# Kernel optimization log

Measured on AMD Instinct MI355X. Metric: run time of the kernel, lower is better.

The kernel has to match this reference:

```python
import jax, jax.numpy as jnp
import numpy as np

EMBED_DIM = 1024
NUM_HEADS = 16
HEAD_DIM = EMBED_DIM // NUM_HEADS
B, S = 4, 2048


def setup_inputs() -> dict:
    key = jax.random.key(0)
    k1, k2, k3, k4, k5 = jax.random.split(key, 5)
    x = jax.random.normal(k1, (B, S, EMBED_DIM), dtype=jnp.float32)
    # torch nn.Linear params: W [out, in], b [out]; init scale ~ 1/sqrt(in)
    s = 1.0 / np.sqrt(EMBED_DIM)
    qkv_w = jax.random.uniform(k2, (3 * EMBED_DIM, EMBED_DIM), jnp.float32, -s, s)
    qkv_b = jax.random.uniform(k3, (3 * EMBED_DIM,), jnp.float32, -s, s)
    out_w = jax.random.uniform(k4, (EMBED_DIM, EMBED_DIM), jnp.float32, -s, s)
    out_b = jax.random.uniform(k5, (EMBED_DIM,), jnp.float32, -s, s)
    return {"x": x, "qkv_w": qkv_w, "qkv_b": qkv_b, "out_w": out_w, "out_b": out_b}


def reference(x, qkv_w, qkv_b, out_w, out_b):
    b, s, e = x.shape
    # qkv: [B,S,3E]
    qkv = x @ qkv_w.T + qkv_b
    # Faithful to source: reshape to [B,S,H,3*hd] then transpose -> [B,H,S,3*hd]
    qkv = qkv.reshape(b, s, NUM_HEADS, 3 * HEAD_DIM).transpose(0, 2, 1, 3)
    q, k, v = jnp.split(qkv, 3, axis=-1)  # each [B,H,S,hd]
    q = q / np.sqrt(HEAD_DIM).astype(np.float32)
    scores = jnp.einsum('bhqd,bhkd->bhqk', q, k)  # [B,H,S,S]
    attn = jax.nn.softmax(scores, axis=-1)
    out = jnp.einsum('bhqk,bhkd->bhqd', attn, v)  # [B,H,S,hd]
    out = out.transpose(0, 2, 1, 3).reshape(b, s, e)
    return out @ out_w.T + out_b
```

## Files before the change

### kernel.cpp

```cpp
#include <hip/hip_runtime.h>

#define EMBED   1024
#define THREE_E 3072
#define NHEAD   16
#define HDIM    64
#define BATCH   4
#define SEQ     2048
#define MTOK    (BATCH * SEQ)
#define QKW     2048

typedef __attribute__((ext_vector_type(8))) _Float16 half8;
typedef __attribute__((ext_vector_type(4))) _Float16 half4;
typedef __attribute__((ext_vector_type(4))) float    f32x4;

#define QSCALE 0.18033688011112042f

__device__ inline f32x4 mfma16(half8 a, half8 b, f32x4 c) {
    return __builtin_amdgcn_mfma_f32_16x16x32_f16(a, b, c, 0, 0, 0);
}
__device__ inline f32x4 mfma16k16(half4 a, half4 b, f32x4 c) {
    return __builtin_amdgcn_mfma_f32_16x16x16f16(a, b, c, 0, 0, 0);
}

__device__ inline float exp2x(float x) {
    float r;
    asm("v_exp_f32 %0, %1" : "=v"(r) : "v"(x));
    return r;
}

__device__ inline void gld16(const void* g, void* l) {
    __builtin_amdgcn_global_load_lds(
        (const __attribute__((address_space(1))) unsigned*)g,
        (__attribute__((address_space(3))) unsigned*)l, 16, 0, 0);
}

__global__ __launch_bounds__(256) void tohi_kernel(const float* __restrict__ in,
                                                   _Float16* __restrict__ hi, int n)
{
    int i = (blockIdx.x * 256 + threadIdx.x) << 2;
    if (i < n) {
        const float4 v = *(const float4*)(in + i);
        half4 h;
        h[0] = (_Float16)v.x; h[1] = (_Float16)v.y;
        h[2] = (_Float16)v.z; h[3] = (_Float16)v.w;
        *(half4*)(hi + i) = h;
    }
}

template<int OMODE>
__global__ __launch_bounds__(256) void gemm_mfma_nt(
    const _Float16* __restrict__ Ahi,
    const _Float16* __restrict__ Bhi,
    const float*  __restrict__ bias,
    float* __restrict__ Cf,
    _Float16* __restrict__ QKhi,
    _Float16* __restrict__ Vthi,
    int N, int K)
{
    __shared__ __align__(16) _Float16 sA[2][8][64][8];
    __shared__ __align__(16) _Float16 sB[2][8][64][8];

    const int tid  = threadIdx.x;
    const int w    = tid >> 6;
    const int lane = tid & 63;
    const int quad = lane >> 4;
    const int c    = lane & 15;
    const int wm   = w >> 1, wn = w & 1;

    const int gx   = gridDim.x;
    const int nwg  = gx * gridDim.y;
    const int lin0 = blockIdx.y * gx + blockIdx.x;
    const int wg   = (lin0 & 7) * (nwg >> 3) + (lin0 >> 3);
    const int m0   = (wg / gx) << 7;
    const int n0   = (wg % gx) << 7;

    f32x4 acc[4][4];
#pragma unroll
    for (int i = 0; i < 4; ++i)
#pragma unroll
        for (int j = 0; j < 4; ++j) acc[i][j] = (f32x4){0.f, 0.f, 0.f, 0.f};

    const _Float16* ap0 = Ahi + (size_t)(m0 + (w << 4)       + c) * K + (quad << 3);
    const _Float16* ap1 = Ahi + (size_t)(m0 + ((4 + w) << 4) + c) * K + (quad << 3);
    const _Float16* bp0 = Bhi + (size_t)(n0 + (w << 4)       + c) * K + (quad << 3);
    const _Float16* bp1 = Bhi + (size_t)(n0 + ((4 + w) << 4) + c) * K + (quad << 3);

    auto stage = [&](int bfs) {
        gld16(ap0, &sA[bfs][w][0][0]);
        gld16(ap1, &sA[bfs][4 + w][0][0]);
        gld16(bp0, &sB[bfs][w][0][0]);
        gld16(bp1, &sB[bfs][4 + w][0][0]);
        ap0 += 32; ap1 += 32; bp0 += 32; bp1 += 32;
    };

    stage(0);
    int bf = 0;
    for (int k0 = 0; k0 < K; k0 += 32) {
        __syncthreads();
        if (k0 + 32 < K) stage(bf ^ 1);

        half8 aH[4], bH[4];
#pragma unroll
        for (int i = 0; i < 4; ++i) {
            aH[i] = *(const half8*)&sA[bf][(wm << 2) + i][lane][0];
            bH[i] = *(const half8*)&sB[bf][(wn << 2) + i][lane][0];
        }
#pragma unroll
        for (int i = 0; i < 4; ++i)
#pragma unroll
            for (int j = 0; j < 4; ++j)
                acc[i][j] = mfma16(aH[i], bH[j], acc[i][j]);
        bf ^= 1;
    }

#pragma unroll
    for (int j = 0; j < 4; ++j) {
        const int n  = n0 + (wn << 6) + (j << 4) + c;
        const float bb = bias[n];
        const int h  = n / 192;
        const int rem = n - h * 192;
#pragma unroll
        for (int i = 0; i < 4; ++i) {
            const int mb = m0 + (wm << 6) + (i << 4) + (quad << 2);
            if constexpr (OMODE == 0) {
#pragma unroll
                for (int r = 0; r < 4; ++r)
                    Cf[(size_t)(mb + r) * N + n] = acc[i][j][r] + bb;
            } else {
                if (rem < 128) {
                    const size_t col = h * 128 + rem;
                    const float scale = (rem < 64) ? QSCALE : 1.0f;
#pragma unroll
                    for (int r = 0; r < 4; ++r)
                        QKhi[(size_t)(mb + r) * QKW + col] =
                            (_Float16)((acc[i][j][r] + bb) * scale);
                } else {
                    const int d = rem - 128;
                    const int b = mb >> 11;
                    const int s = mb & 2047;
                    half4 h4;
#pragma unroll
                    for (int r = 0; r < 4; ++r)
                        h4[r] = (_Float16)(acc[i][j][r] + bb);
                    const size_t off = ((size_t)(h * 64 + d) * BATCH + b) * SEQ + s;
                    *(half4*)(Vthi + off) = h4;
                }
            }
        }
    }
}

__global__ __launch_bounds__(256, 4) void attn_mfma(
    const _Float16* __restrict__ qkhi,
    const _Float16* __restrict__ vthi,
    _Float16* __restrict__ attnf)
{
    __shared__ __align__(16) _Float16 Kf[2][8][512];
    __shared__ __align__(16) _Float16 Vf[2][8][512];

    const int tid  = threadIdx.x;
    const int w    = tid >> 6;
    const int lane = tid & 63;
    const int quad = lane >> 4;
    const int c    = lane & 15;

    const int lin = blockIdx.x;
    const int g   = lin & 7;
    const int s   = lin >> 3;
    const int bh  = g * 8 + (s >> 4);
    const int qt  = s & 15;
    const int b   = bh >> 4, h = bh & 15;
    const int q0  = qt * 128;

    const size_t bSEQ  = (size_t)b * SEQ;
    const int    qcol  = h * 128;
    const int    kcol  = h * 128 + 64;
    const size_t vbase = ((size_t)(h * 64) * BATCH + b) * SEQ;

    half8 qh[2][2];
#pragma unroll
    for (int t = 0; t < 2; ++t) {
        const size_t row = (bSEQ + q0 + w * 32 + t * 16 + c) * QKW;
#pragma unroll
        for (int ks = 0; ks < 2; ++ks)
            qh[t][ks] = *(const half8*)(qkhi + row + qcol + ks * 32 + quad * 8);
    }

    f32x4 lacc[2];
    f32x4 oacc[4][2];
#pragma unroll
    for (int t = 0; t < 2; ++t) {
        lacc[t] = (f32x4){0.f, 0.f, 0.f, 0.f};
#pragma unroll
        for (int v = 0; v < 4; ++v) oacc[v][t] = (f32x4){0.f, 0.f, 0.f, 0.f};
    }

    const half4 one4 = {(_Float16)1.f, (_Float16)1.f, (_Float16)1.f, (_Float16)1.f};

    const int ku0 = w >> 1,       kks0 = w & 1;
    const int ku1 = (4 + w) >> 1, kks1 = (4 + w) & 1;
    const _Float16* kp0 = qkhi + (bSEQ + ku0 * 16 + c) * QKW + kcol + kks0 * 32 + quad * 8;
    const _Float16* kp1 = qkhi + (bSEQ + ku1 * 16 + c) * QKW + kcol + kks1 * 32 + quad * 8;
    const int lswz = lane ^ ((((lane >> 3) & 1) << 1) | (((lane >> 4) & 1) << 2));
    const int qs   = lswz >> 4, cs = lswz & 15;
    const _Float16* vp0 = vthi + vbase + (size_t)(ku0 * 16 + cs) * (BATCH * SEQ) + kks0 * 32 + qs * 8;
    const _Float16* vp1 = vthi + vbase + (size_t)(ku1 * 16 + cs) * (BATCH * SEQ) + kks1 * 32 + qs * 8;

    auto stageKV = [&](int bfs) {
        gld16(kp0, &Kf[bfs][w][0]);
        gld16(kp1, &Kf[bfs][4 + w][0]);
        gld16(vp0, &Vf[bfs][w][0]);
        gld16(vp1, &Vf[bfs][4 + w][0]);
        kp0 += 64 * QKW; kp1 += 64 * QKW; vp0 += 64; vp1 += 64;
    };

    stageKV(0);
    int bf = 0;

    for (int kt = 0; kt < SEQ / 64; ++kt) {
        __syncthreads();
        if (kt + 1 < SEQ / 64) stageKV(bf ^ 1);

        f32x4 sacc[2][4];
        __builtin_amdgcn_s_setprio(1);
#pragma unroll
        for (int u = 0; u < 4; ++u) {
            const half8 kh0 = *(const half8*)&Kf[bf][(u << 1) + 0][lane << 3];
            const half8 kh1 = *(const half8*)&Kf[bf][(u << 1) + 1][lane << 3];
#pragma unroll
            for (int t = 0; t < 2; ++t) {
                f32x4 a = (f32x4){0.f, 0.f, 0.f, 0.f};
                a = mfma16(kh0, qh[t][0], a);
                a = mfma16(kh1, qh[t][1], a);
                sacc[t][u] = a;
            }
        }
        __builtin_amdgcn_s_setprio(0);

        half4 pk[2][4];
#pragma unroll
        for (int t = 0; t < 2; ++t)
#pragma unroll
            for (int u = 0; u < 4; ++u) {
                const float p0 = exp2x(sacc[t][u][0]);
                const float p1 = exp2x(sacc[t][u][1]);
                const float p2 = exp2x(sacc[t][u][2]);
                const float p3 = exp2x(sacc[t][u][3]);
                const auto lo = __builtin_amdgcn_cvt_pkrtz(p0, p1);
                const auto hi = __builtin_amdgcn_cvt_pkrtz(p2, p3);
                half4 pp;
                pp[0] = (_Float16)lo[0]; pp[1] = (_Float16)lo[1];
                pp[2] = (_Float16)hi[0]; pp[3] = (_Float16)hi[1];
                pk[t][u] = pp;
            }

        half4 va[4][4];
#pragma unroll
        for (int v = 0; v < 4; ++v)
#pragma unroll
            for (int u = 0; u < 4; ++u) {
                const int qp   = ((u & 1) << 1) + (quad >> 1);
                int elem = ((qp << 4) + c) * 8 + ((quad & 1) << 2);
                elem ^= (((c >> 3) & 1) << 4) ^ ((qp & 1) << 5);
                va[v][u] = *(const half4*)&Vf[bf][(v << 1) + (u >> 1)][elem];
            }

        __builtin_amdgcn_s_setprio(1);
#pragma unroll
        for (int t = 0; t < 2; ++t) {
#pragma unroll
            for (int v = 0; v < 4; ++v) {
                f32x4 a = oacc[v][t];
#pragma unroll
                for (int u = 0; u < 4; ++u)
                    a = mfma16k16(va[v][u], pk[t][u], a);
                oacc[v][t] = a;
            }
            f32x4 l = lacc[t];
#pragma unroll
            for (int u = 0; u < 4; ++u)
                l = mfma16k16(one4, pk[t][u], l);
            lacc[t] = l;
        }
        __builtin_amdgcn_s_setprio(0);

        bf ^= 1;
    }

#pragma unroll
    for (int t = 0; t < 2; ++t) {
        const float inv = 1.0f / lacc[t][0];
        const int tok = q0 + w * 32 + t * 16 + c;
#pragma unroll
        for (int v = 0; v < 4; ++v) {
            half4 o;
#pragma unroll
            for (int r = 0; r < 4; ++r) o[r] = (_Float16)(oacc[v][t][r] * inv);
            *(half4*)&attnf[(bSEQ + tok) * EMBED + h * HDIM + v * 16 + (quad << 2)] = o;
        }
    }
}

extern "C" void kernel_launch(void* const* d_in, const int* in_sizes, int n_in,
                              void* d_out, int out_size, void* d_ws, size_t ws_size,
                              hipStream_t stream)
{
    const float* x     = (const float*)d_in[0];
    const float* qkv_w = (const float*)d_in[1];
    const float* qkv_b = (const float*)d_in[2];
    const float* out_w = (const float*)d_in[3];
    const float* out_b = (const float*)d_in[4];

    _Float16* qkhi  = (_Float16*)d_ws;
    _Float16* vthi  = qkhi  + (size_t)MTOK * QKW;
    _Float16* w1hi  = vthi  + (size_t)NHEAD * HDIM * BATCH * SEQ;
    _Float16* w2hi  = w1hi  + (size_t)THREE_E * EMBED;
    _Float16* attnf = w2hi  + (size_t)EMBED * EMBED;

    _Float16* xhi = (_Float16*)d_out;

    tohi_kernel<<<(MTOK * EMBED / 4 + 255) / 256, 256, 0, stream>>>(x, xhi, MTOK * EMBED);
    tohi_kernel<<<(THREE_E * EMBED / 4 + 255) / 256, 256, 0, stream>>>(qkv_w, w1hi, THREE_E * EMBED);
    tohi_kernel<<<(EMBED * EMBED / 4 + 255) / 256, 256, 0, stream>>>(out_w, w2hi, EMBED * EMBED);

    gemm_mfma_nt<1><<<dim3(THREE_E / 128, MTOK / 128), 256, 0, stream>>>(
        xhi, w1hi, qkv_b, nullptr, qkhi, vthi, THREE_E, EMBED);

    attn_mfma<<<dim3(1024), 256, 0, stream>>>(qkhi, vthi, attnf);

    gemm_mfma_nt<0><<<dim3(EMBED / 128, MTOK / 128), 256, 0, stream>>>(
        attnf, w2hi, out_b, (float*)d_out, nullptr, nullptr, EMBED, EMBED);
}
```

Measured before the change: 325.1 us.

## Use 128x256 eight-wave GEMM tiles with K=64 staging and merge fp16 casts

Both projection GEMMs now use 512-thread blocks computing 128x256 tiles, staging 64-wide K slices and splitting each step into two halves with barriers, interleaved prefetches and raised MFMA priority. The aim is more operand reuse per LDS load and better overlap of global-to-LDS copies with compute. The three fp32-to-fp16 conversion launches are merged into one kernel to cut launch overhead. In exchange, LDS use per block rises and fewer blocks are launched, notably only 256 for the output projection, which may leave CUs underused.

Result: faster. 316.1 us (-2.8%).

```diff
diff --git a/kernel.cpp b/kernel.cpp
--- a/kernel.cpp
+++ b/kernel.cpp
@@ -34,21 +34,26 @@
         (__attribute__((address_space(3))) unsigned*)l, 16, 0, 0);
 }
 
-__global__ __launch_bounds__(256) void tohi_kernel(const float* __restrict__ in,
-                                                   _Float16* __restrict__ hi, int n)
+__global__ __launch_bounds__(256) void tohi3_kernel(
+    const float* __restrict__ x,  _Float16* __restrict__ xo,
+    const float* __restrict__ w1, _Float16* __restrict__ w1o,
+    const float* __restrict__ w2, _Float16* __restrict__ w2o)
 {
-    int i = (blockIdx.x * 256 + threadIdx.x) << 2;
-    if (i < n) {
-        const float4 v = *(const float4*)(in + i);
-        half4 h;
-        h[0] = (_Float16)v.x; h[1] = (_Float16)v.y;
-        h[2] = (_Float16)v.z; h[3] = (_Float16)v.w;
-        *(half4*)(hi + i) = h;
-    }
+    const int bid = blockIdx.x;
+    const float* src; _Float16* dst; int base;
+    if (bid < 8192)             { src = x;  dst = xo;  base = bid * 1024; }
+    else if (bid < 8192 + 3072) { src = w1; dst = w1o; base = (bid - 8192) * 1024; }
+    else                        { src = w2; dst = w2o; base = (bid - 11264) * 1024; }
+    const int i = base + (threadIdx.x << 2);
+    const float4 v = *(const float4*)(src + i);
+    half4 h;
+    h[0] = (_Float16)v.x; h[1] = (_Float16)v.y;
+    h[2] = (_Float16)v.z; h[3] = (_Float16)v.w;
+    *(half4*)(dst + i) = h;
 }
 
 template<int OMODE>
-__global__ __launch_bounds__(256) void gemm_mfma_nt(
+__global__ __launch_bounds__(512, 2) void gemm_big(
     const _Float16* __restrict__ Ahi,
     const _Float16* __restrict__ Bhi,
     const float*  __restrict__ bias,
@@ -57,22 +62,22 @@
     _Float16* __restrict__ Vthi,
     int N, int K)
 {
-    __shared__ __align__(16) _Float16 sA[2][8][64][8];
-    __shared__ __align__(16) _Float16 sB[2][8][64][8];
+    __shared__ __align__(16) _Float16 sA[2][8][2][64][8];
+    __shared__ __align__(16) _Float16 sB[2][16][2][64][8];
 
     const int tid  = threadIdx.x;
     const int w    = tid >> 6;
     const int lane = tid & 63;
     const int quad = lane >> 4;
     const int c    = lane & 15;
-    const int wm   = w >> 1, wn = w & 1;
+    const int wr   = w >> 2, wc = w & 3;
 
     const int gx   = gridDim.x;
     const int nwg  = gx * gridDim.y;
     const int lin0 = blockIdx.y * gx + blockIdx.x;
     const int wg   = (lin0 & 7) * (nwg >> 3) + (lin0 >> 3);
     const int m0   = (wg / gx) << 7;
-    const int n0   = (wg % gx) << 7;
+    const int n0   = (wg % gx) << 8;
 
     f32x4 acc[4][4];
 #pragma unroll
@@ -80,52 +85,88 @@
 #pragma unroll
         for (int j = 0; j < 4; ++j) acc[i][j] = (f32x4){0.f, 0.f, 0.f, 0.f};
 
-    const _Float16* ap0 = Ahi + (size_t)(m0 + (w << 4)       + c) * K + (quad << 3);
-    const _Float16* ap1 = Ahi + (size_t)(m0 + ((4 + w) << 4) + c) * K + (quad << 3);
-    const _Float16* bp0 = Bhi + (size_t)(n0 + (w << 4)       + c) * K + (quad << 3);
-    const _Float16* bp1 = Bhi + (size_t)(n0 + ((4 + w) << 4) + c) * K + (quad << 3);
-
-    auto stage = [&](int bfs) {
-        gld16(ap0, &sA[bfs][w][0][0]);
-        gld16(ap1, &sA[bfs][4 + w][0][0]);
-        gld16(bp0, &sB[bfs][w][0][0]);
-        gld16(bp1, &sB[bfs][4 + w][0][0]);
-        ap0 += 32; ap1 += 32; bp0 += 32; bp1 += 32;
-    };
-
-    stage(0);
-    int bf = 0;
-    for (int k0 = 0; k0 < K; k0 += 32) {
-        __syncthreads();
-        if (k0 + 32 < K) stage(bf ^ 1);
-
-        half8 aH[4], bH[4];
-#pragma unroll
-        for (int i = 0; i < 4; ++i) {
-            aH[i] = *(const half8*)&sA[bf][(wm << 2) + i][lane][0];
-            bH[i] = *(const half8*)&sB[bf][(wn << 2) + i][lane][0];
-        }
-#pragma unroll
-        for (int i = 0; i < 4; ++i)
-#pragma unroll
-            for (int j = 0; j < 4; ++j)
-                acc[i][j] = mfma16(aH[i], bH[j], acc[i][j]);
-        bf ^= 1;
-    }
-
-#pragma unroll
-    for (int j = 0; j < 4; ++j) {
-        const int n  = n0 + (wn << 6) + (j << 4) + c;
+    const int rg0 = w >> 1, ksb = w & 1;
+    const size_t sK64 = (size_t)64 * K;
+    const _Float16* ap = Ahi + (size_t)(m0 + rg0 * 16 + c) * K + ksb * 32 + quad * 8;
+    const _Float16* bp = Bhi + (size_t)(n0 + rg0 * 16 + c) * K + ksb * 32 + quad * 8;
+
+    gld16(ap,            &sA[0][rg0][ksb][0][0]);
+    gld16(ap + sK64,     &sA[0][4 + rg0][ksb][0][0]);
+    gld16(bp,            &sB[0][rg0][ksb][0][0]);
+    gld16(bp + sK64,     &sB[0][4 + rg0][ksb][0][0]);
+    gld16(bp + 2 * sK64, &sB[0][8 + rg0][ksb][0][0]);
+    gld16(bp + 3 * sK64, &sB[0][12 + rg0][ksb][0][0]);
+    ap += 64; bp += 64;
+
+    const int NT = K >> 6;
+    for (int t = 0; t < NT; ++t) {
+        const int slot = t & 1;
+        asm volatile("s_waitcnt vmcnt(0)" ::: "memory");
+        asm volatile("s_barrier" ::: "memory");
+        const bool pre = (t + 1) < NT;
+
+        half8 aH[4][2], bH[4][2];
+#pragma unroll
+        for (int fr = 0; fr < 4; ++fr)
+#pragma unroll
+            for (int ks = 0; ks < 2; ++ks)
+                aH[fr][ks] = *(const half8*)&sA[slot][wr * 4 + fr][ks][lane][0];
+#pragma unroll
+        for (int fc = 0; fc < 2; ++fc)
+#pragma unroll
+            for (int ks = 0; ks < 2; ++ks)
+                bH[fc][ks] = *(const half8*)&sB[slot][wc * 4 + fc][ks][lane][0];
+        if (pre) {
+            gld16(ap,        &sA[slot ^ 1][rg0][ksb][0][0]);
+            gld16(ap + sK64, &sA[slot ^ 1][4 + rg0][ksb][0][0]);
+            gld16(bp,        &sB[slot ^ 1][rg0][ksb][0][0]);
+        }
+        __builtin_amdgcn_s_setprio(1);
+#pragma unroll
+        for (int fr = 0; fr < 4; ++fr)
+#pragma unroll
+            for (int fc = 0; fc < 2; ++fc)
+#pragma unroll
+                for (int ks = 0; ks < 2; ++ks)
+                    acc[fr][fc] = mfma16(aH[fr][ks], bH[fc][ks], acc[fr][fc]);
+        __builtin_amdgcn_s_setprio(0);
+        asm volatile("s_barrier" ::: "memory");
+
+#pragma unroll
+        for (int fc = 2; fc < 4; ++fc)
+#pragma unroll
+            for (int ks = 0; ks < 2; ++ks)
+                bH[fc][ks] = *(const half8*)&sB[slot][wc * 4 + fc][ks][lane][0];
+        if (pre) {
+            gld16(bp + sK64,     &sB[slot ^ 1][4 + rg0][ksb][0][0]);
+            gld16(bp + 2 * sK64, &sB[slot ^ 1][8 + rg0][ksb][0][0]);
+            gld16(bp + 3 * sK64, &sB[slot ^ 1][12 + rg0][ksb][0][0]);
+            ap += 64; bp += 64;
+        }
+        __builtin_amdgcn_s_setprio(1);
+#pragma unroll
+        for (int fr = 0; fr < 4; ++fr)
+#pragma unroll
+            for (int fc = 2; fc < 4; ++fc)
+#pragma unroll
+                for (int ks = 0; ks < 2; ++ks)
+                    acc[fr][fc] = mfma16(aH[fr][ks], bH[fc][ks], acc[fr][fc]);
+        __builtin_amdgcn_s_setprio(0);
+    }
+
+#pragma unroll
+    for (int fc = 0; fc < 4; ++fc) {
+        const int n  = n0 + wc * 64 + fc * 16 + c;
         const float bb = bias[n];
         const int h  = n / 192;
         const int rem = n - h * 192;
 #pragma unroll
-        for (int i = 0; i < 4; ++i) {
-            const int mb = m0 + (wm << 6) + (i << 4) + (quad << 2);
+        for (int fr = 0; fr < 4; ++fr) {
+            const int mb = m0 + wr * 64 + fr * 16 + (quad << 2);
             if constexpr (OMODE == 0) {
 #pragma unroll
                 for (int r = 0; r < 4; ++r)
-                    Cf[(size_t)(mb + r) * N + n] = acc[i][j][r] + bb;
+                    Cf[(size_t)(mb + r) * N + n] = acc[fr][fc][r] + bb;
             } else {
                 if (rem < 128) {
                     const size_t col = h * 128 + rem;
@@ -133,7 +174,7 @@
 #pragma unroll
                     for (int r = 0; r < 4; ++r)
                         QKhi[(size_t)(mb + r) * QKW + col] =
-                            (_Float16)((acc[i][j][r] + bb) * scale);
+                            (_Float16)((acc[fr][fc][r] + bb) * scale);
                 } else {
                     const int d = rem - 128;
                     const int b = mb >> 11;
@@ -141,7 +182,7 @@
                     half4 h4;
 #pragma unroll
                     for (int r = 0; r < 4; ++r)
-                        h4[r] = (_Float16)(acc[i][j][r] + bb);
+                        h4[r] = (_Float16)(acc[fr][fc][r] + bb);
                     const size_t off = ((size_t)(h * 64 + d) * BATCH + b) * SEQ + s;
                     *(half4*)(Vthi + off) = h4;
                 }
@@ -319,15 +360,13 @@
 
     _Float16* xhi = (_Float16*)d_out;
 
-    tohi_kernel<<<(MTOK * EMBED / 4 + 255) / 256, 256, 0, stream>>>(x, xhi, MTOK * EMBED);
-    tohi_kernel<<<(THREE_E * EMBED / 4 + 255) / 256, 256, 0, stream>>>(qkv_w, w1hi, THREE_E * EMBED);
-    tohi_kernel<<<(EMBED * EMBED / 4 + 255) / 256, 256, 0, stream>>>(out_w, w2hi, EMBED * EMBED);
-
-    gemm_mfma_nt<1><<<dim3(THREE_E / 128, MTOK / 128), 256, 0, stream>>>(
+    tohi3_kernel<<<dim3(12288), 256, 0, stream>>>(x, xhi, qkv_w, w1hi, out_w, w2hi);
+
+    gemm_big<1><<<dim3(THREE_E / 256, MTOK / 128), 512, 0, stream>>>(
         xhi, w1hi, qkv_b, nullptr, qkhi, vthi, THREE_E, EMBED);
 
     attn_mfma<<<dim3(1024), 256, 0, stream>>>(qkhi, vthi, attnf);
 
-    gemm_mfma_nt<0><<<dim3(EMBED / 128, MTOK / 128), 256, 0, stream>>>(
+    gemm_big<0><<<dim3(EMBED / 256, MTOK / 128), 512, 0, stream>>>(
         attnf, w2hi, out_b, (float*)d_out, nullptr, nullptr, EMBED, EMBED);
 }
```
